# Kernel optimization log

Measured on AMD Instinct MI355X. Metric: run time of the kernel, lower is better.

Reference implementation:

```python
import jax, jax.numpy as jnp
import numpy as np

HIDDEN = 2048
N_HEADS = 16
HEAD_DIM = HIDDEN // N_HEADS
BATCH = 2
SEQ = 2048
N_CP = max(8, int(HIDDEN * HIDDEN / 128.9))  # 32540 control points


def _spline_to_weight(cp, out_dim, in_dim):
    # Reconstruct full weight matrix by sampling the control-point curve at
    # out_dim*in_dim evenly spaced parameter values (piecewise-linear spline eval).
    n = cp.shape[0]
    t = jnp.linspace(0.0, 1.0, out_dim * in_dim)
    xp = jnp.linspace(0.0, 1.0, n)
    return jnp.interp(t, xp, cp).reshape(out_dim, in_dim)


def setup_inputs() -> dict:
    key = jax.random.key(0)
    ks = jax.random.split(key, 5)
    hidden_states = jax.random.normal(ks[0], (BATCH, SEQ, HIDDEN), dtype=jnp.float32)
    cp_q = jax.random.normal(ks[1], (N_CP,), dtype=jnp.float32) * 0.02
    cp_k = jax.random.normal(ks[2], (N_CP,), dtype=jnp.float32) * 0.02
    cp_v = jax.random.normal(ks[3], (N_CP,), dtype=jnp.float32) * 0.02
    cp_o = jax.random.normal(ks[4], (N_CP,), dtype=jnp.float32) * 0.02
    # additive causal mask [1,1,S,S]
    causal = jnp.tril(jnp.ones((SEQ, SEQ), dtype=bool))
    attention_mask = jnp.where(causal, 0.0, -1e9).astype(jnp.float32)[None, None]
    return {
        'hidden_states': hidden_states,
        'cp_q': cp_q, 'cp_k': cp_k, 'cp_v': cp_v, 'cp_o': cp_o,
        'attention_mask': attention_mask,
    }


def reference(hidden_states, cp_q, cp_k, cp_v, cp_o, attention_mask):
    B, S, H = hidden_states.shape
    q_w = _spline_to_weight(cp_q, H, H)
    k_w = _spline_to_weight(cp_k, H, H)
    v_w = _spline_to_weight(cp_v, H, H)
    o_w = _spline_to_weight(cp_o, H, H)

    # F.linear(x, W) == x @ W.T
    q = (hidden_states @ q_w.T).reshape(B, S, N_HEADS, HEAD_DIM).transpose(0, 2, 1, 3)
    k = (hidden_states @ k_w.T).reshape(B, S, N_HEADS, HEAD_DIM).transpose(0, 2, 1, 3)
    v = (hidden_states @ v_w.T).reshape(B, S, N_HEADS, HEAD_DIM).transpose(0, 2, 1, 3)

    scale = 1.0 / np.sqrt(HEAD_DIM).astype(np.float32)
    scores = jnp.einsum('bhqd,bhkd->bhqk', q, k) * scale + attention_mask
    probs = jax.nn.softmax(scores.astype(jnp.float32), axis=-1).astype(q.dtype)
    attn = jnp.einsum('bhqk,bhkd->bhqd', probs, v)
    attn = attn.transpose(0, 2, 1, 3).reshape(B, S, H)
    return attn @ o_w.T
```

## Files before the change

kernel.cpp:

```cpp
#include <hip/hip_runtime.h>
#include <stdint.h>

typedef unsigned short u16;
typedef __bf16 bf16x8 __attribute__((ext_vector_type(8)));
typedef float f32x4 __attribute__((ext_vector_type(4)));
typedef u16 u16x4 __attribute__((ext_vector_type(4)));

#define MFMA16(a, b, c) __builtin_amdgcn_mfma_f32_16x16x32_bf16((a), (b), (c), 0, 0, 0)

__device__ __forceinline__ u16 f2bf(float f) {
  uint32_t u = __builtin_bit_cast(uint32_t, f);
  u += 0x7FFFu + ((u >> 16) & 1u);
  return (u16)(u >> 16);
}
__device__ __forceinline__ bf16x8 cvt8(f32x4 lo, f32x4 hi) {
  union { u16 u[8]; bf16x8 v; } r;
#pragma unroll
  for (int j = 0; j < 4; j++) { r.u[j] = f2bf(lo[j]); r.u[4 + j] = f2bf(hi[j]); }
  return r.v;
}
__device__ __forceinline__ void gld_lds16(const void* g, void* l) {
  __builtin_amdgcn_global_load_lds(
      (const __attribute__((address_space(1))) uint32_t*)g,
      (__attribute__((address_space(3))) uint32_t*)l, 16, 0, 0);
}

__global__ void prep_kernel(const float* __restrict__ x, const float* __restrict__ cpq,
                            const float* __restrict__ cpk, const float* __restrict__ cpv,
                            const float* __restrict__ cpo, u16* __restrict__ xb,
                            u16* __restrict__ Wqkv, u16* __restrict__ Wo,
                            int n, double factor) {
  int blk = blockIdx.x;
  if (blk < 8192) {
    int base = (blk * 256 + threadIdx.x) * 8;
    int w = base >> 22;
    int i = base & 4194303;
    const float* cp = (w == 0) ? cpq : (w == 1) ? cpk : (w == 2) ? cpv : cpo;
    union { u16 u[8]; bf16x8 v; } r;
#pragma unroll
    for (int s = 0; s < 8; s++) {
      double u = (double)(i + s) * factor;
      int i0 = (int)u;
      if (i0 > n - 2) i0 = n - 2;
      float fr = (float)(u - (double)i0);
      float f0 = cp[i0], f1 = cp[i0 + 1];
      r.u[s] = f2bf(f0 + fr * (f1 - f0));
    }
    if (w < 3) *(bf16x8*)(Wqkv + base) = r.v;
    else       *(bf16x8*)(Wo + i) = r.v;
  } else {
    size_t i = ((size_t)(blk - 8192) * 256 + threadIdx.x) * 8;
    const f32x4* p = (const f32x4*)(x + i);
    *(bf16x8*)(xb + i) = cvt8(p[0], p[1]);
  }
}

template <int MODE>
__global__ __launch_bounds__(256, 2)
void gemm_bt(const u16* __restrict__ A, const u16* __restrict__ B,
             u16* __restrict__ oQ, u16* __restrict__ oK, u16* __restrict__ oV,
             float* __restrict__ oC) {
  constexpr int KD = 2048;
  __shared__ __align__(16) u16 As[128 * 64];
  __shared__ __align__(16) u16 Bs[128 * 64];
  const int tid = threadIdx.x;
  const int wave = tid >> 6, lane = tid & 63, quad = lane >> 4, l16 = lane & 15;
  const int wm = wave & 1, wn = wave >> 1;
  const int m0 = blockIdx.y * 128, n0 = blockIdx.x * 128;

  size_t aoff[4], boff[4];
  int lslot[4];
#pragma unroll
  for (int b = 0; b < 4; b++) {
    int s = wave * 256 + b * 64 + lane;
    int r = s >> 3, c = s & 7, gc = c ^ (r & 7);
    lslot[b] = s * 16;
    aoff[b] = (size_t)(m0 + r) * (KD * 2) + gc * 16;
    boff[b] = (size_t)(n0 + r) * (KD * 2) + gc * 16;
  }
  const char* Ab = (const char*)A;
  const char* Bb = (const char*)B;
  char* AsB = (char*)As;
  char* BsB = (char*)Bs;

  f32x4 acc[4][4];
  const f32x4 fz = {0.f, 0.f, 0.f, 0.f};
#pragma unroll
  for (int i = 0; i < 4; i++)
#pragma unroll
    for (int j = 0; j < 4; j++) acc[i][j] = fz;

  for (int kt = 0; kt < KD / 64; ++kt) {
    if (kt) __syncthreads();
#pragma unroll
    for (int b = 0; b < 4; b++) {
      gld_lds16(Ab + aoff[b], AsB + lslot[b]);
      gld_lds16(Bb + boff[b], BsB + lslot[b]);
      aoff[b] += 128;
      boff[b] += 128;
    }
    __syncthreads();
#pragma unroll
    for (int t = 0; t < 2; t++) {
      bf16x8 af[4], bfb[4];
#pragma unroll
      for (int i = 0; i < 4; i++) {
        int row = wm * 64 + i * 16 + l16;
        int ch = (t * 4 + quad) ^ (row & 7);
        af[i] = *(const bf16x8*)(AsB + row * 128 + ch * 16);
      }
#pragma unroll
      for (int j = 0; j < 4; j++) {
        int row = wn * 64 + j * 16 + l16;
        int ch = (t * 4 + quad) ^ (row & 7);
        bfb[j] = *(const bf16x8*)(BsB + row * 128 + ch * 16);
      }
#pragma unroll
      for (int i = 0; i < 4; i++)
#pragma unroll
        for (int j = 0; j < 4; j++) acc[i][j] = MFMA16(af[i], bfb[j], acc[i][j]);
    }
  }

  if (MODE == 0) {
    const float qscale = 0.08838834764831845f;
#pragma unroll
    for (int j = 0; j < 4; j++) {
      int nb = n0 + wn * 64 + j * 16;
      int sel = nb >> 11;
      int h = (nb >> 7) & 15;
      int d = (nb & 127) + l16;
#pragma unroll
      for (int i = 0; i < 4; i++) {
        int mrow = m0 + wm * 64 + i * 16 + quad * 4;
        int bq = mrow >> 11, srow = mrow & 2047;
        if (sel == 2) {
          u16x4 pk = {f2bf(acc[i][j][0]), f2bf(acc[i][j][1]),
                      f2bf(acc[i][j][2]), f2bf(acc[i][j][3])};
          *(u16x4*)&oV[(size_t)(((bq << 4) + h) * 128 + d) * 2048 + srow] = pk;
        } else if (sel == 0) {
          int base = ((bq << 4) + h) * 2048;
#pragma unroll
          for (int r = 0; r < 4; r++)
            oQ[(size_t)(base + srow + r) * 128 + d] = f2bf(acc[i][j][r] * qscale);
        } else {
          int base = ((bq << 4) + h) * 2048;
#pragma unroll
          for (int r = 0; r < 4; r++)
            oK[(size_t)(base + srow + r) * 128 + d] = f2bf(acc[i][j][r]);
        }
      }
    }
  } else {
#pragma unroll
    for (int j = 0; j < 4; j++) {
      int col = n0 + wn * 64 + j * 16 + l16;
#pragma unroll
      for (int i = 0; i < 4; i++) {
        int mrow = m0 + wm * 64 + i * 16 + quad * 4;
#pragma unroll
        for (int r = 0; r < 4; r++) oC[(size_t)(mrow + r) * 2048 + col] = acc[i][j][r];
      }
    }
  }
}

__global__ __launch_bounds__(256, 2)
void flash_attn(const u16* __restrict__ Q, const u16* __restrict__ Kg,
                const u16* __restrict__ Vt, u16* __restrict__ attn) {
  __shared__ __align__(16) u16 Ks[64 * 128];
  __shared__ __align__(16) u16 Vs[128 * 64];
  __shared__ __align__(16) u16 Ps[128 * 72];
  const int tid = threadIdx.x;
  const int wave = tid >> 6, lane = tid & 63, quad = lane >> 4, l16 = lane & 15;
  const int L = blockIdx.x;
  const int g = L >> 3;
  const int s4 = g >> 2;
  const int qt = (s4 < 8) ? s4 : 23 - s4;
  const int bh = (L & 7) * 4 + (g & 3);
  const int q0 = qt * 128;
  const u16* Qb = Q + (size_t)bh * 2048 * 128;
  const u16* Kb = Kg + (size_t)bh * 2048 * 128;
  const u16* Vb = Vt + (size_t)bh * 128 * 2048;

  bf16x8 qf[2][4];
#pragma unroll
  for (int i = 0; i < 2; i++) {
    int row = q0 + wave * 32 + i * 16 + l16;
#pragma unroll
    for (int t = 0; t < 4; t++)
      qf[i][t] = *(const bf16x8*)(Qb + (size_t)row * 128 + t * 32 + quad * 8);
  }

  f32x4 o_acc[2][8];
  const f32x4 fz = {0.f, 0.f, 0.f, 0.f};
#pragma unroll
  for (int i = 0; i < 2; i++)
#pragma unroll
    for (int j = 0; j < 8; j++) o_acc[i][j] = fz;
  float l_i[2] = {0.f, 0.f};

  int koff[4], voff[4], lslot[4];
#pragma unroll
  for (int b = 0; b < 4; b++) {
    int s = wave * 256 + b * 64 + lane;
    lslot[b] = s * 16;
    {
      int r = s >> 4, c = s & 15;
      int gc = (c & 8) | ((c & 7) ^ (r & 7));
      koff[b] = r * 256 + gc * 16;
    }
    {
      int r = s >> 3, c = s & 7;
      int gc = c ^ (r & 7);
      voff[b] = r * 4096 + gc * 16;
    }
  }
  const char* KbB = (const char*)Kb;
  const char* VbB = (const char*)Vb;
  char* KsB = (char*)Ks;
  char* VsB = (char*)Vs;

  const int ktmax = 2 * qt + 1;

  for (int kt = 0; kt <= ktmax; ++kt) {
    const int k0 = kt * 64;
    if (kt) __syncthreads();
#pragma unroll
    for (int b = 0; b < 4; b++) {
      gld_lds16(KbB + (size_t)k0 * 256 + koff[b], KsB + lslot[b]);
      gld_lds16(VbB + (size_t)k0 * 2 + voff[b], VsB + lslot[b]);
    }
    __syncthreads();

    f32x4 st[2][4];
#pragma unroll
    for (int i = 0; i < 2; i++)
#pragma unroll
      for (int j = 0; j < 4; j++) st[i][j] = fz;
#pragma unroll
    for (int j = 0; j < 4; j++) {
      int rowk = j * 16 + l16;
#pragma unroll
      for (int t = 0; t < 4; t++) {
        int cc = t * 4 + quad;
        int ch = (cc & 8) | ((cc & 7) ^ (rowk & 7));
        bf16x8 kfr = *(const bf16x8*)(KsB + rowk * 256 + ch * 16);
        st[0][j] = MFMA16(kfr, qf[0][t], st[0][j]);
        st[1][j] = MFMA16(kfr, qf[1][t], st[1][j]);
      }
    }

    const bool do_mask = (kt >= 2 * qt);
#pragma unroll
    for (int i = 0; i < 2; i++) {
      const int qg = q0 + wave * 32 + i * 16 + l16;
      float lacc = 0.f;
#pragma unroll
      for (int j = 0; j < 4; j++) {
        float p[4];
#pragma unroll
        for (int r = 0; r < 4; r++) {
          float v = st[i][j][r];
          if (do_mask && (k0 + j * 16 + quad * 4 + r > qg)) v = -1e30f;
          p[r] = __expf(v);
        }
        lacc += (p[0] + p[1]) + (p[2] + p[3]);
        u16x4 pk = {f2bf(p[0]), f2bf(p[1]), f2bf(p[2]), f2bf(p[3])};
        *(u16x4*)&Ps[(wave * 32 + i * 16 + l16) * 72 + j * 16 + quad * 4] = pk;
      }
      l_i[i] += lacc;
    }

#pragma unroll
    for (int t = 0; t < 2; t++) {
      bf16x8 af0 = *(const bf16x8*)((char*)Ps + (wave * 32 + l16) * 144 + (t * 32 + quad * 8) * 2);
      bf16x8 af1 = *(const bf16x8*)((char*)Ps + (wave * 32 + 16 + l16) * 144 + (t * 32 + quad * 8) * 2);
#pragma unroll
      for (int j = 0; j < 8; j++) {
        int vrow = j * 16 + l16;
        int ch = (t * 4 + quad) ^ (vrow & 7);
        bf16x8 bfr = *(const bf16x8*)(VsB + vrow * 128 + ch * 16);
        o_acc[0][j] = MFMA16(af0, bfr, o_acc[0][j]);
        o_acc[1][j] = MFMA16(af1, bfr, o_acc[1][j]);
      }
    }
  }

  const int bb = bh >> 4, h = bh & 15;
#pragma unroll
  for (int i = 0; i < 2; i++) {
    float rs = l_i[i];
    rs += __shfl_xor(rs, 16);
    rs += __shfl_xor(rs, 32);
    float inv = 1.f / rs;
#pragma unroll
    for (int r = 0; r < 4; r++) {
      float invr = __shfl(inv, (lane & 48) | (quad * 4 + r), 64);
      int srow = q0 + wave * 32 + i * 16 + quad * 4 + r;
      size_t base = ((size_t)(bb * 2048 + srow)) * 2048 + h * 128;
#pragma unroll
      for (int j = 0; j < 8; j++) attn[base + j * 16 + l16] = f2bf(o_acc[i][j][r] * invr);
    }
  }
}

extern "C" void kernel_launch(void* const* d_in, const int* in_sizes, int n_in,
                              void* d_out, int out_size, void* d_ws, size_t ws_size,
                              hipStream_t stream) {
  (void)n_in; (void)out_size; (void)ws_size;
  const float* x = (const float*)d_in[0];
  const float* cpq = (const float*)d_in[1];
  const float* cpk = (const float*)d_in[2];
  const float* cpv = (const float*)d_in[3];
  const float* cpo = (const float*)d_in[4];
  float* out = (float*)d_out;
  const int ncp = in_sizes[1];
  const double factor = (double)(ncp - 1) / 4194303.0;

  char* ws = (char*)d_ws;
  u16* Wqkv = (u16*)(ws);
  u16* At   = (u16*)(ws);
  u16* Wo = (u16*)(ws + 25165824);
  u16* Qp = (u16*)(ws + 33554432);
  u16* Kp = (u16*)(ws + 50331648);
  u16* Vp = (u16*)(ws + 67108864);
  u16* xb = (u16*)d_out;

  prep_kernel<<<dim3(12288), dim3(256), 0, stream>>>(x, cpq, cpk, cpv, cpo, xb, Wqkv, Wo, ncp, factor);
  gemm_bt<0><<<dim3(48, 32), dim3(256), 0, stream>>>(xb, Wqkv, Qp, Kp, Vp, nullptr);
  flash_attn<<<dim3(512), dim3(256), 0, stream>>>(Qp, Kp, Vp, At);
  gemm_bt<1><<<dim3(16, 32), dim3(256), 0, stream>>>(At, Wo, nullptr, nullptr, nullptr, out);
}
```

Before: 325.2 us.

## Read K and V fragments directly from global memory instead of staging through LDS

Removes the LDS staging buffers for K and V tiles in the flash attention kernel, along with both block-wide barriers per key tile. Each wave now loads its MFMA operand fragments straight from global memory (via L1/L2), avoiding the barriers and the LDS footprint. The cost is that all four waves redundantly fetch the same K/V data from global or cache with no prefetch overlap, which adds latency and memory traffic per tile.

```diff
diff --git a/kernel.cpp b/kernel.cpp
--- a/kernel.cpp
+++ b/kernel.cpp
@@ -168,8 +168,6 @@
 __global__ __launch_bounds__(256, 2)
 void flash_attn(const u16* __restrict__ Q, const u16* __restrict__ Kg,
                 const u16* __restrict__ Vt, u16* __restrict__ attn) {
-  __shared__ __align__(16) u16 Ks[64 * 128];
-  __shared__ __align__(16) u16 Vs[128 * 64];
   __shared__ __align__(16) u16 Ps[128 * 72];
   const int tid = threadIdx.x;
   const int wave = tid >> 6, lane = tid & 63, quad = lane >> 4, l16 = lane & 15;
@@ -200,38 +198,13 @@
     for (int j = 0; j < 8; j++) o_acc[i][j] = fz;
   float l_i[2] = {0.f, 0.f};
 
-  int koff[4], voff[4], lslot[4];
-#pragma unroll
-  for (int b = 0; b < 4; b++) {
-    int s = wave * 256 + b * 64 + lane;
-    lslot[b] = s * 16;
-    {
-      int r = s >> 4, c = s & 15;
-      int gc = (c & 8) | ((c & 7) ^ (r & 7));
-      koff[b] = r * 256 + gc * 16;
-    }
-    {
-      int r = s >> 3, c = s & 7;
-      int gc = c ^ (r & 7);
-      voff[b] = r * 4096 + gc * 16;
-    }
-  }
   const char* KbB = (const char*)Kb;
   const char* VbB = (const char*)Vb;
-  char* KsB = (char*)Ks;
-  char* VsB = (char*)Vs;
 
   const int ktmax = 2 * qt + 1;
 
   for (int kt = 0; kt <= ktmax; ++kt) {
     const int k0 = kt * 64;
-    if (kt) __syncthreads();
-#pragma unroll
-    for (int b = 0; b < 4; b++) {
-      gld_lds16(KbB + (size_t)k0 * 256 + koff[b], KsB + lslot[b]);
-      gld_lds16(VbB + (size_t)k0 * 2 + voff[b], VsB + lslot[b]);
-    }
-    __syncthreads();
 
     f32x4 st[2][4];
 #pragma unroll
@@ -240,12 +213,10 @@
       for (int j = 0; j < 4; j++) st[i][j] = fz;
 #pragma unroll
     for (int j = 0; j < 4; j++) {
-      int rowk = j * 16 + l16;
+      const char* Krow = KbB + (size_t)(k0 + j * 16 + l16) * 256;
 #pragma unroll
       for (int t = 0; t < 4; t++) {
-        int cc = t * 4 + quad;
-        int ch = (cc & 8) | ((cc & 7) ^ (rowk & 7));
-        bf16x8 kfr = *(const bf16x8*)(KsB + rowk * 256 + ch * 16);
+        bf16x8 kfr = *(const bf16x8*)(Krow + (t * 4 + quad) * 16);
         st[0][j] = MFMA16(kfr, qf[0][t], st[0][j]);
         st[1][j] = MFMA16(kfr, qf[1][t], st[1][j]);
       }
@@ -276,11 +247,10 @@
     for (int t = 0; t < 2; t++) {
       bf16x8 af0 = *(const bf16x8*)((char*)Ps + (wave * 32 + l16) * 144 + (t * 32 + quad * 8) * 2);
       bf16x8 af1 = *(const bf16x8*)((char*)Ps + (wave * 32 + 16 + l16) * 144 + (t * 32 + quad * 8) * 2);
+      const char* Vcol = VbB + (size_t)(k0 + t * 32 + quad * 8) * 2;
 #pragma unroll
       for (int j = 0; j < 8; j++) {
-        int vrow = j * 16 + l16;
-        int ch = (t * 4 + quad) ^ (vrow & 7);
-        bf16x8 bfr = *(const bf16x8*)(VsB + vrow * 128 + ch * 16);
+        bf16x8 bfr = *(const bf16x8*)(Vcol + (size_t)(j * 16 + l16) * 4096);
         o_acc[0][j] = MFMA16(af0, bfr, o_acc[0][j]);
         o_acc[1][j] = MFMA16(af1, bfr, o_acc[1][j]);
       }
```

Result: slower. 371.7 us (+14.3%).
